# Performance work log

Measured on AMD Instinct MI355X. Metric: run time of the kernel, lower is better.

The kernel has to match this reference:

```python
import jax, jax.numpy as jnp
import numpy as np

B, T = 4096, 16384

def setup_inputs() -> dict:
    key = jax.random.key(0)
    ks = jax.random.split(key, 6)
    x = jax.random.normal(ks[0], (B, T), dtype=jnp.float32)
    v0 = jnp.zeros((B, 2), dtype=jnp.float32)
    # match torch init ranges: b* ~ U(-1,1), a* ~ U(-0.5,0.5) (stable region)
    b0 = jax.random.uniform(ks[1], (1,), jnp.float32, -1.0, 1.0)
    b1 = jax.random.uniform(ks[2], (1,), jnp.float32, -1.0, 1.0)
    b2 = jax.random.uniform(ks[3], (1,), jnp.float32, -1.0, 1.0)
    a1 = jax.random.uniform(ks[4], (1,), jnp.float32, -0.5, 0.5)
    a2 = jax.random.uniform(ks[5], (1,), jnp.float32, -0.5, 0.5)
    return {"x": x, "v0": v0, "b0": b0, "b1": b1, "b2": b2, "a1": a1, "a2": a2}

def reference(x, v0, b0, b1, b2, a1, a2):
    """DF-II transposed biquad, scanned over time.
    x: [B, T] input samples; v0: [B, 2] initial state.
    Returns (y [B, T], v_final [B, 2]).
    Per-step math is exactly DTDFIICell.forward:
      y   = x_t * b0 + v[:,0]
      v0' = x_t * b1 + v[:,1] - y * a1
      v1' = x_t * b2            - y * a2
    """
    def step(v, xt):  # v: [B,2], xt: [B]
        y = xt * b0 + v[:, 0]                      # [B]
        v_new = jnp.stack(
            [xt * b1 + v[:, 1] - y * a1,
             xt * b2 - y * a2], axis=-1)           # [B,2]
        return v_new, y
    v_final, ys = jax.lax.scan(step, v0, x.T)      # ys: [T, B]
    return ys.T, v_final
```

## Files before the change

kernel.cpp:

```cpp
#include <hip/hip_runtime.h>

#define B_DIM 4096
#define T_DIM 16384
#define WAVES_PER_BLOCK 4
#define PER_LANE 8
#define CHUNK (64 * PER_LANE)
#define NIT (T_DIM / CHUNK)
#define VSTEP (CHUNK / 4)

typedef float f32x4 __attribute__((ext_vector_type(4)));

struct M2 { float a, b, c, d; };

__device__ inline M2 m2mul(const M2& X, const M2& Y) {
    M2 r;
    r.a = fmaf(X.a, Y.a, X.b * Y.c);
    r.b = fmaf(X.a, Y.b, X.b * Y.d);
    r.c = fmaf(X.c, Y.a, X.d * Y.c);
    r.d = fmaf(X.c, Y.b, X.d * Y.d);
    return r;
}

__global__ __launch_bounds__(256) void biquad_scan_kernel(
    const float* __restrict__ x, const float* __restrict__ v0in,
    const float* __restrict__ pb0, const float* __restrict__ pb1,
    const float* __restrict__ pb2, const float* __restrict__ pa1,
    const float* __restrict__ pa2,
    float* __restrict__ y, float* __restrict__ vout)
{
    const int lane = threadIdx.x & 63;
    const int wave = threadIdx.x >> 6;
    const int row  = blockIdx.x * WAVES_PER_BLOCK + wave;
    if (row >= B_DIM) return;

    const float b0 = *pb0, b1 = *pb1, b2 = *pb2, a1 = *pa1, a2 = *pa2;
    const float na1 = -a1, na2 = -a2;
    const float c0 = b1 - a1 * b0;
    const float c1 = b2 - a2 * b0;

    M2 A  { na1, 1.0f, na2, 0.0f };
    M2 A2 = m2mul(A, A);
    M2 A4 = m2mul(A2, A2);
    M2 A8 = m2mul(A4, A4);

    M2 S0, S1, S2, S3, S4, S5;
    M2 Q { 1.f, 0.f, 0.f, 1.f };
    M2 M = A8;
    S0 = M; if (lane & 1)  Q = m2mul(M, Q); M = m2mul(M, M);
    S1 = M; if (lane & 2)  Q = m2mul(M, Q); M = m2mul(M, M);
    S2 = M; if (lane & 4)  Q = m2mul(M, Q); M = m2mul(M, M);
    S3 = M; if (lane & 8)  Q = m2mul(M, Q); M = m2mul(M, M);
    S4 = M; if (lane & 16) Q = m2mul(M, Q); M = m2mul(M, M);
    S5 = M; if (lane & 32) Q = m2mul(M, Q); M = m2mul(M, M);
    const M2 R = M;

    const float* xr = x + (size_t)row * T_DIM;
    float*       yr = y + (size_t)row * T_DIM;

    float vc0 = v0in[row * 2 + 0];
    float vc1 = v0in[row * 2 + 1];

    const f32x4* xp = (const f32x4*)xr + 2 * lane;
    f32x4*       yp = (f32x4*)yr + 2 * lane;

    f32x4 xa  = xp[0],     xb  = xp[1];
    f32x4 nxa = xp[VSTEP], nxb = xp[VSTEP + 1];

    for (int i = 0; i < NIT; ++i) {
        f32x4 mxa = {0.f, 0.f, 0.f, 0.f}, mxb = {0.f, 0.f, 0.f, 0.f};
        if (i + 2 < NIT) {
            mxa = xp[(size_t)(i + 2) * VSTEP];
            mxb = xp[(size_t)(i + 2) * VSTEP + 1];
        }

        float d0 = c0 * xa[0];
        float d1 = c1 * xa[0];
        #define FOLD(xs)                                               \
        {   float t0 = fmaf(c0, (xs), fmaf(na1, d0, d1));              \
            float t1 = fmaf(na2, d0, c1 * (xs));                       \
            d0 = t0; d1 = t1; }
        FOLD(xa[1]) FOLD(xa[2]) FOLD(xa[3])
        FOLD(xb[0]) FOLD(xb[1]) FOLD(xb[2]) FOLD(xb[3])
        #undef FOLD

        #define SCAN_STEP(Sm, o)                                        \
        {   float q0 = __shfl_up(d0, (unsigned)(o));                    \
            float q1 = __shfl_up(d1, (unsigned)(o));                    \
            if (lane < (o)) { q0 = 0.f; q1 = 0.f; }                     \
            float t0 = fmaf(Sm.a, q0, fmaf(Sm.b, q1, d0));              \
            float t1 = fmaf(Sm.c, q0, fmaf(Sm.d, q1, d1));              \
            d0 = t0; d1 = t1; }
        SCAN_STEP(S0, 1)
        SCAN_STEP(S1, 2)
        SCAN_STEP(S2, 4)
        SCAN_STEP(S3, 8)
        SCAN_STEP(S4, 16)
        SCAN_STEP(S5, 32)
        #undef SCAN_STEP

        float e0 = __shfl_up(d0, 1u);
        float e1 = __shfl_up(d1, 1u);
        if (lane == 0) { e0 = 0.f; e1 = 0.f; }

        float v0r = fmaf(Q.a, vc0, fmaf(Q.b, vc1, e0));
        float v1r = fmaf(Q.c, vc0, fmaf(Q.d, vc1, e1));

        f32x4 yo0, yo1;
        #define REPLAY(xs, dst)                                        \
        {   float yy = fmaf((xs), b0, v0r);                            \
            float n0 = fmaf(na1, yy, fmaf((xs), b1, v1r));             \
            float n1 = fmaf(na2, yy, (xs) * b2);                       \
            v0r = n0; v1r = n1; dst = yy; }
        REPLAY(xa[0], yo0[0]) REPLAY(xa[1], yo0[1])
        REPLAY(xa[2], yo0[2]) REPLAY(xa[3], yo0[3])
        REPLAY(xb[0], yo1[0]) REPLAY(xb[1], yo1[1])
        REPLAY(xb[2], yo1[2]) REPLAY(xb[3], yo1[3])
        #undef REPLAY

        yp[(size_t)i * VSTEP]     = yo0;
        yp[(size_t)i * VSTEP + 1] = yo1;

        float t0 = __shfl(d0, 63);
        float t1 = __shfl(d1, 63);
        float nv0 = fmaf(R.a, vc0, fmaf(R.b, vc1, t0));
        float nv1 = fmaf(R.c, vc0, fmaf(R.d, vc1, t1));
        vc0 = nv0; vc1 = nv1;

        xa = nxa; xb = nxb; nxa = mxa; nxb = mxb;
    }

    if (lane == 0) {
        vout[row * 2 + 0] = vc0;
        vout[row * 2 + 1] = vc1;
    }
}

extern "C" void kernel_launch(void* const* d_in, const int* in_sizes, int n_in,
                              void* d_out, int out_size, void* d_ws, size_t ws_size,
                              hipStream_t stream) {
    const float* x   = (const float*)d_in[0];
    const float* v0  = (const float*)d_in[1];
    const float* b0  = (const float*)d_in[2];
    const float* b1  = (const float*)d_in[3];
    const float* b2  = (const float*)d_in[4];
    const float* a1  = (const float*)d_in[5];
    const float* a2  = (const float*)d_in[6];

    float* y    = (float*)d_out;
    float* vout = (float*)d_out + (size_t)B_DIM * T_DIM;

    dim3 grid(B_DIM / WAVES_PER_BLOCK);
    dim3 block(64 * WAVES_PER_BLOCK);
    biquad_scan_kernel<<<grid, block, 0, stream>>>(x, v0, b0, b1, b2, a1, a2, y, vout);
}
```

Before: 118.5 us.

## Shrink per-lane chunk to 4 samples and use nontemporal loads/stores

Cuts each lane's per-iteration work from 8 samples to 4, so one 16-byte vector per lane is contiguous across the wave, and rebases the scan matrices on A^4. It also switches x loads and y stores to nontemporal builtins so the streamed data bypasses cache retention. The trade-off is twice as many iterations, with the full 6-step shuffle scan and carry propagation now done per 256 samples rather than 512, which adds serial latency and shuffle overhead per sample.

```diff
diff --git a/kernel.cpp b/kernel.cpp
--- a/kernel.cpp
+++ b/kernel.cpp
@@ -3,10 +3,8 @@
 #define B_DIM 4096
 #define T_DIM 16384
 #define WAVES_PER_BLOCK 4
-#define PER_LANE 8
-#define CHUNK (64 * PER_LANE)
+#define CHUNK 256
 #define NIT (T_DIM / CHUNK)
-#define VSTEP (CHUNK / 4)
 
 typedef float f32x4 __attribute__((ext_vector_type(4)));
 
@@ -41,11 +39,10 @@
     M2 A  { na1, 1.0f, na2, 0.0f };
     M2 A2 = m2mul(A, A);
     M2 A4 = m2mul(A2, A2);
-    M2 A8 = m2mul(A4, A4);
 
     M2 S0, S1, S2, S3, S4, S5;
     M2 Q { 1.f, 0.f, 0.f, 1.f };
-    M2 M = A8;
+    M2 M = A4;
     S0 = M; if (lane & 1)  Q = m2mul(M, Q); M = m2mul(M, M);
     S1 = M; if (lane & 2)  Q = m2mul(M, Q); M = m2mul(M, M);
     S2 = M; if (lane & 4)  Q = m2mul(M, Q); M = m2mul(M, M);
@@ -60,27 +57,24 @@
     float vc0 = v0in[row * 2 + 0];
     float vc1 = v0in[row * 2 + 1];
 
-    const f32x4* xp = (const f32x4*)xr + 2 * lane;
-    f32x4*       yp = (f32x4*)yr + 2 * lane;
+    const f32x4* xp = (const f32x4*)xr;
+    f32x4*       yp = (f32x4*)yr;
 
-    f32x4 xa  = xp[0],     xb  = xp[1];
-    f32x4 nxa = xp[VSTEP], nxb = xp[VSTEP + 1];
+    f32x4 xv = __builtin_nontemporal_load(&xp[lane]);
+    f32x4 xn = __builtin_nontemporal_load(&xp[64 + lane]);
 
     for (int i = 0; i < NIT; ++i) {
-        f32x4 mxa = {0.f, 0.f, 0.f, 0.f}, mxb = {0.f, 0.f, 0.f, 0.f};
-        if (i + 2 < NIT) {
-            mxa = xp[(size_t)(i + 2) * VSTEP];
-            mxb = xp[(size_t)(i + 2) * VSTEP + 1];
-        }
+        f32x4 xm = {0.f, 0.f, 0.f, 0.f};
+        if (i + 2 < NIT)
+            xm = __builtin_nontemporal_load(&xp[(size_t)(i + 2) * 64 + lane]);
 
-        float d0 = c0 * xa[0];
-        float d1 = c1 * xa[0];
+        float d0 = c0 * xv[0];
+        float d1 = c1 * xv[0];
         #define FOLD(xs)                                               \
         {   float t0 = fmaf(c0, (xs), fmaf(na1, d0, d1));              \
             float t1 = fmaf(na2, d0, c1 * (xs));                       \
             d0 = t0; d1 = t1; }
-        FOLD(xa[1]) FOLD(xa[2]) FOLD(xa[3])
-        FOLD(xb[0]) FOLD(xb[1]) FOLD(xb[2]) FOLD(xb[3])
+        FOLD(xv[1]) FOLD(xv[2]) FOLD(xv[3])
         #undef FOLD
 
         #define SCAN_STEP(Sm, o)                                        \
@@ -105,20 +99,17 @@
         float v0r = fmaf(Q.a, vc0, fmaf(Q.b, vc1, e0));
         float v1r = fmaf(Q.c, vc0, fmaf(Q.d, vc1, e1));
 
-        f32x4 yo0, yo1;
+        f32x4 yv;
         #define REPLAY(xs, dst)                                        \
         {   float yy = fmaf((xs), b0, v0r);                            \
             float n0 = fmaf(na1, yy, fmaf((xs), b1, v1r));             \
             float n1 = fmaf(na2, yy, (xs) * b2);                       \
             v0r = n0; v1r = n1; dst = yy; }
-        REPLAY(xa[0], yo0[0]) REPLAY(xa[1], yo0[1])
-        REPLAY(xa[2], yo0[2]) REPLAY(xa[3], yo0[3])
-        REPLAY(xb[0], yo1[0]) REPLAY(xb[1], yo1[1])
-        REPLAY(xb[2], yo1[2]) REPLAY(xb[3], yo1[3])
+        REPLAY(xv[0], yv[0]) REPLAY(xv[1], yv[1])
+        REPLAY(xv[2], yv[2]) REPLAY(xv[3], yv[3])
         #undef REPLAY
 
-        yp[(size_t)i * VSTEP]     = yo0;
-        yp[(size_t)i * VSTEP + 1] = yo1;
+        __builtin_nontemporal_store(yv, &yp[(size_t)i * 64 + lane]);
 
         float t0 = __shfl(d0, 63);
         float t1 = __shfl(d1, 63);
@@ -126,7 +117,7 @@
         float nv1 = fmaf(R.c, vc0, fmaf(R.d, vc1, t1));
         vc0 = nv0; vc1 = nv1;
 
-        xa = nxa; xb = nxb; nxa = mxa; nxb = mxb;
+        xv = xn; xn = xm;
     }
 
     if (lane == 0) {
```

After: 121.0 us. +2.1%, slower.
